# Optimization experiments

Hardware: AMD Instinct MI355X
Metric: run time of the kernel (lower is better)

Reference implementation:

```python
import jax, jax.numpy as jnp
import numpy as np

N_HEADS = 16

def _rope_tables(L, head_dim, dtype):
    inv_freq = 1.0 / (10000.0 ** (jnp.arange(0, head_dim, 2, dtype=jnp.float32) / head_dim))
    t = jnp.arange(L, dtype=jnp.float32)
    freqs = jnp.outer(t, inv_freq)            # [L, head_dim/2]
    emb = jnp.concatenate([freqs, freqs], -1)  # [L, head_dim]
    return jnp.cos(emb).astype(dtype), jnp.sin(emb).astype(dtype)

def _apply_rope(x, cos, sin):
    # x: [B, L, H, hd]; cos/sin: [1, L, 1, hd]
    half = x.shape[-1] // 2
    x1, x2 = x[..., :half], x[..., half:]
    x_rot = jnp.concatenate([-x2, x1], -1)
    return x * cos + x_rot * sin

def setup_inputs() -> dict:
    key = jax.random.key(0)
    ks = jax.random.split(key, 5)
    D = 1024
    s = 0.02
    return {
        "x": jax.random.normal(ks[0], (4, 2048, D), jnp.float32),
        "w_qkv": jax.random.normal(ks[1], (3 * D, D), jnp.float32) * s,
        "b_qkv": jax.random.normal(ks[2], (3 * D,), jnp.float32) * s,
        "w_out": jax.random.normal(ks[3], (D, D), jnp.float32) * s,
        "b_out": jax.random.normal(ks[4], (D,), jnp.float32) * s,
    }

def reference(x, w_qkv, b_qkv, w_out, b_out):
    B, L, D = x.shape
    H = N_HEADS
    hd = D // H
    scale = hd ** -0.5
    qkv = (x @ w_qkv.T + b_qkv).reshape(B, L, 3, H, hd)
    q, k, v = qkv[:, :, 0], qkv[:, :, 1], qkv[:, :, 2]  # [B,L,H,hd]
    cos, sin = _rope_tables(L, hd, x.dtype)
    cos = cos[None, :, None, :]
    sin = sin[None, :, None, :]
    q = _apply_rope(q, cos, sin)
    k = _apply_rope(k, cos, sin)
    # [B,H,L,L] scores, non-causal softmax
    attn = jnp.einsum('blhd,bmhd->bhlm', q, k) * scale
    attn = jax.nn.softmax(attn, axis=-1)
    out = jnp.einsum('bhlm,bmhd->blhd', attn, v).reshape(B, L, D)
    return out @ w_out.T + b_out
```

## Files before the change

### kernel.cpp

```cpp
#include <hip/hip_runtime.h>
#include <stdint.h>

typedef __attribute__((ext_vector_type(4))) float f32x4;
typedef __attribute__((ext_vector_type(8))) short bf16x8;
typedef __attribute__((ext_vector_type(4))) short s16x4;
typedef __attribute__((ext_vector_type(4))) float fp32x4;

#define QSCALE 0.18033688f

__device__ __forceinline__ short f2bf(float f) {
    union { float f; unsigned u; } v; v.f = f;
    unsigned u = v.u;
    unsigned r = u + 0x7fffu + ((u >> 16) & 1u);
    return (short)(r >> 16);
}
__device__ __forceinline__ unsigned cvtpk(float a, float b) {
    unsigned r;
    asm("v_cvt_pk_bf16_f32 %0, %1, %2" : "=v"(r) : "v"(a), "v"(b));
    return r;
}

__device__ __forceinline__ void gld_lds16(const void* g, void* l) {
    __builtin_amdgcn_global_load_lds(
        (const __attribute__((address_space(1))) unsigned int*)(uintptr_t)g,
        (__attribute__((address_space(3))) unsigned int*)(uintptr_t)l,
        16, 0, 0);
}

__global__ __launch_bounds__(256) void cast_kernel(const float* __restrict__ in,
                                                   short* __restrict__ out, int n) {
    int idx = (blockIdx.x * 256 + threadIdx.x) * 8;
    if (idx >= n) return;
    fp32x4 a = *(const fp32x4*)&in[idx];
    fp32x4 b = *(const fp32x4*)&in[idx + 4];
    union { unsigned w[4]; bf16x8 v; } u;
    u.w[0] = cvtpk(a[0], a[1]); u.w[1] = cvtpk(a[2], a[3]);
    u.w[2] = cvtpk(b[0], b[1]); u.w[3] = cvtpk(b[2], b[3]);
    *(bf16x8*)&out[idx] = u.v;
}

__global__ __launch_bounds__(256) void rope_table_kernel(float* __restrict__ tab) {
    int idx = blockIdx.x * 256 + threadIdx.x;
    int l = idx >> 5, d = idx & 31;
    float inv = expf(-(float)d / 32.f * logf(10000.f));
    float ang = (float)l * inv;
    tab[idx * 2 + 0] = cosf(ang);
    tab[idx * 2 + 1] = sinf(ang);
}

template<int MODE>
__global__ __launch_bounds__(512, 2) void gemm_bt(const short* __restrict__ A,
                                                  const short* __restrict__ B,
                                                  const float* __restrict__ bias,
                                                  void* __restrict__ Cout,
                                                  short* __restrict__ VTout,
                                                  const float* __restrict__ tab,
                                                  int M, int N, int K) {
    __shared__ short lds[3 * 24576];
    const int tid = threadIdx.x;
    const int lane = tid & 63, wave = tid >> 6;
    const int i15 = lane & 15, g = lane >> 4;
    const int wr = wave >> 1, wc = wave & 1;

    const int nbx = gridDim.x;
    const int nwg = nbx * gridDim.y;
    int bid = blockIdx.y * nbx + blockIdx.x;
    int sw = (bid & 7) * (nwg >> 3) + (bid >> 3);
    const int m0 = (sw / nbx) * 256;
    const int n0 = (sw % nbx) * 128;

    const int xr3 = i15 & 3, xb2 = (i15 >> 2) & 1;
    const int cLo = g ^ xr3;
    const int aoff0 = (wr * 64 + i15) * 64 + (xb2 * 4 + cLo) * 8;
    const int aoff1 = (wr * 64 + i15) * 64 + ((1 ^ xb2) * 4 + cLo) * 8;
    const int boff0 = (wc * 64 + i15) * 64 + (xb2 * 4 + cLo) * 8;
    const int boff1 = (wc * 64 + i15) * 64 + ((1 ^ xb2) * 4 + cLo) * 8;

    const int srow = tid >> 3;
    const int ss = (tid & 7) ^ (srow & 7);
    const short* a0 = A + (size_t)(m0 + srow) * K + ss * 8;
    const short* a1 = a0 + (size_t)64 * K;
    const short* a2 = a0 + (size_t)128 * K;
    const short* a3 = a0 + (size_t)192 * K;
    const short* b0 = B + (size_t)(n0 + srow) * K + ss * 8;
    const short* b1 = b0 + (size_t)64 * K;

#define ST_A(slot, r, p) do { gld_lds16(p, lds + (slot) * 24576 + ((r) * 512 + wave * 64) * 8); p += 64; } while (0)
#define ST_B(slot, r, p) do { gld_lds16(p, lds + (slot) * 24576 + 16384 + ((r) * 512 + wave * 64) * 8); p += 64; } while (0)

    ST_A(0, 0, a0); ST_A(0, 1, a1); ST_B(0, 0, b0);
    ST_A(0, 2, a2); ST_A(0, 3, a3); ST_B(0, 1, b1);
    ST_A(1, 0, a0); ST_A(1, 1, a1); ST_B(1, 0, b0);
    ST_A(1, 2, a2); ST_A(1, 3, a3); ST_B(1, 1, b1);

    f32x4 acc[4][4] = {};
    const int NT = K >> 6;
    int slc = 0;

    for (int t = 0; t < NT; ++t) {
        int sl2 = slc + 2; if (sl2 >= 3) sl2 -= 3;
        if (t == NT - 1) asm volatile("s_waitcnt vmcnt(0)" ::: "memory");
        else             asm volatile("s_waitcnt vmcnt(6)" ::: "memory");
        __builtin_amdgcn_s_barrier();
        __builtin_amdgcn_sched_barrier(0);

        const short* As_ = lds + slc * 24576;
        const short* Bs_ = As_ + 16384;
        const bool pre = (t + 2 < NT);

        if (pre) { ST_A(sl2, 0, a0); ST_A(sl2, 1, a1); ST_B(sl2, 0, b0); }
        bf16x8 af[4][2], bfr[2][2];
#pragma unroll
        for (int m = 0; m < 4; ++m) {
            af[m][0] = *(const bf16x8*)&As_[aoff0 + m * 1024];
            af[m][1] = *(const bf16x8*)&As_[aoff1 + m * 1024];
        }
#pragma unroll
        for (int n = 0; n < 2; ++n) {
            bfr[n][0] = *(const bf16x8*)&Bs_[boff0 + n * 1024];
            bfr[n][1] = *(const bf16x8*)&Bs_[boff1 + n * 1024];
        }
        __builtin_amdgcn_s_barrier();
        asm volatile("s_waitcnt lgkmcnt(0)" ::: "memory");
        __builtin_amdgcn_sched_barrier(0);
        __builtin_amdgcn_s_setprio(1);
#pragma unroll
        for (int m = 0; m < 4; ++m)
#pragma unroll
            for (int n = 0; n < 2; ++n)
#pragma unroll
                for (int ks = 0; ks < 2; ++ks)
                    acc[m][n] = __builtin_amdgcn_mfma_f32_16x16x32_bf16(af[m][ks], bfr[n][ks], acc[m][n], 0, 0, 0);
        __builtin_amdgcn_s_setprio(0);

        if (pre) { ST_A(sl2, 2, a2); ST_A(sl2, 3, a3); ST_B(sl2, 1, b1); }
        bf16x8 bfr2[2][2];
#pragma unroll
        for (int n = 0; n < 2; ++n) {
            bfr2[n][0] = *(const bf16x8*)&Bs_[boff0 + (n + 2) * 1024];
            bfr2[n][1] = *(const bf16x8*)&Bs_[boff1 + (n + 2) * 1024];
        }
        __builtin_amdgcn_s_barrier();
        asm volatile("s_waitcnt lgkmcnt(0)" ::: "memory");
        __builtin_amdgcn_sched_barrier(0);
        __builtin_amdgcn_s_setprio(1);
#pragma unroll
        for (int m = 0; m < 4; ++m)
#pragma unroll
            for (int n = 0; n < 2; ++n)
#pragma unroll
                for (int ks = 0; ks < 2; ++ks)
                    acc[m][n + 2] = __builtin_amdgcn_mfma_f32_16x16x32_bf16(af[m][ks], bfr2[n][ks], acc[m][n + 2], 0, 0, 0);
        __builtin_amdgcn_s_setprio(0);

        slc = (slc == 2) ? 0 : slc + 1;
    }
#undef ST_A
#undef ST_B

    if (MODE == 0) {
#pragma unroll
        for (int m = 0; m < 4; ++m)
#pragma unroll
            for (int n = 0; n < 4; ++n) {
                int col = n0 + wc * 64 + n * 16 + i15;
                float bcol = bias[col];
#pragma unroll
                for (int j = 0; j < 4; ++j) {
                    int row = m0 + wr * 64 + m * 16 + g * 4 + j;
                    ((float*)Cout)[(size_t)row * N + col] = acc[m][n][j] + bcol;
                }
            }
    } else {
        const int sec = n0 >> 10;
        if (sec < 2) {
            const float qs = (sec == 0) ? QSCALE : 1.0f;
            short* out = (short*)Cout;
#pragma unroll
            for (int m = 0; m < 4; ++m) {
#pragma unroll
                for (int pp = 0; pp < 2; ++pp) {
                    int d = pp * 16 + i15;
                    int collo = n0 + wc * 64 + pp * 16 + i15;
                    float blo = bias[collo], bhi = bias[collo + 32];
#pragma unroll
                    for (int j = 0; j < 4; ++j) {
                        int row = m0 + wr * 64 + m * 16 + g * 4 + j;
                        int l = row & 2047;
                        float2 cs = *(const float2*)&tab[(l * 32 + d) * 2];
                        float x1 = acc[m][pp][j] + blo;
                        float x2 = acc[m][pp + 2][j] + bhi;
                        out[(size_t)row * 3072 + collo]      = f2bf((x1 * cs.x - x2 * cs.y) * qs);
                        out[(size_t)row * 3072 + collo + 32] = f2bf((x2 * cs.x + x1 * cs.y) * qs);
                    }
                }
            }
        } else {
#pragma unroll
            for (int m = 0; m < 4; ++m) {
                int rbase = m0 + wr * 64 + m * 16 + g * 4;
                int lbase = rbase & 2047, bidx = rbase >> 11;
#pragma unroll
                for (int n = 0; n < 4; ++n) {
                    int vcol = (n0 - 2048) + wc * 64 + n * 16 + i15;
                    int h = vcol >> 6, d = vcol & 63;
                    float bb = bias[n0 + wc * 64 + n * 16 + i15];
                    union { unsigned w[2]; s16x4 v; } u;
                    u.w[0] = cvtpk(acc[m][n][0] + bb, acc[m][n][1] + bb);
                    u.w[1] = cvtpk(acc[m][n][2] + bb, acc[m][n][3] + bb);
                    *(s16x4*)&VTout[((size_t)(bidx * 16 + h) * 64 + d) * 2048 + lbase] = u.v;
                }
            }
        }
    }
}

__global__ __launch_bounds__(512, 8) void attn_kernel(const short* __restrict__ qkv,
                                                      const short* __restrict__ VT,
                                                      short* __restrict__ O) {
    __shared__ short Ks[2][64 * 64];
    __shared__ short Vs[2][64 * 64];
    int orig = blockIdx.x;
    int xcd = orig & 7, idx = orig >> 3;
    int bh = xcd * 8 + (idx >> 4), qt = idx & 15;
    int b = bh >> 4, h = bh & 15;
    int tid = threadIdx.x, lane = tid & 63, wave = tid >> 6;
    int i15 = lane & 15, g = lane >> 4;
    int q0 = qt * 128;

    size_t qrow = (size_t)(b * 2048 + q0 + wave * 16 + i15);
    bf16x8 qf[2];
    qf[0] = *(const bf16x8*)&qkv[qrow * 3072 + h * 64 + 0  + g * 8];
    qf[1] = *(const bf16x8*)&qkv[qrow * 3072 + h * 64 + 32 + g * 8];

    bf16x8 onesf;
#pragma unroll
    for (int e = 0; e < 8; ++e) onesf[e] = (short)0x3F80;

    const int srow = tid >> 3, ss8 = (tid & 7) ^ (srow & 7);
    const int sprow = (srow & 0x23) | ((srow & 0x10) >> 2) | ((srow & 0x0C) << 1);
    const short* kp = qkv + (size_t)(b * 2048) * 3072 + 1024 + h * 64
                      + (size_t)sprow * 3072 + ss8 * 8;
    const short* vp = VT + (size_t)bh * 64 * 2048 + (size_t)srow * 2048 + ss8 * 8;

    const int xr3 = i15 & 3, xb2 = (i15 >> 2) & 1;
    const int cLo = g ^ xr3;
    const int o0 = i15 * 64 + (xb2 * 4 + cLo) * 8;
    const int o1 = i15 * 64 + ((1 ^ xb2) * 4 + cLo) * 8;

    f32x4 acc_o[4] = {};
    f32x4 acc_l = {0.f, 0.f, 0.f, 0.f};

#define STAGE(bk, bv)                                        \
    do {                                                     \
        gld_lds16(kp, (bk) + wave * 512);                    \
        gld_lds16(vp, (bv) + wave * 512);                    \
        kp += 64 * 3072;                                     \
        vp += 64;                                            \
    } while (0)

    STAGE(Ks[0], Vs[0]);

    for (int t = 0; t < 32; ++t) {
        const int cur = t & 1;
        if (t > 0) {
            __builtin_amdgcn_s_barrier();
            __builtin_amdgcn_sched_barrier(0);
        }
        if (t + 1 < 32) {
            STAGE(Ks[cur ^ 1], Vs[cur ^ 1]);
            asm volatile("s_waitcnt vmcnt(2)" ::: "memory");
        } else {
            asm volatile("s_waitcnt vmcnt(0)" ::: "memory");
        }
        __builtin_amdgcn_s_barrier();
        __builtin_amdgcn_sched_barrier(0);

        const short* ks = Ks[cur];
        const short* vs = Vs[cur];

        f32x4 sa[4] = {};
        __builtin_amdgcn_s_setprio(1);
#pragma unroll
        for (int kb = 0; kb < 2; ++kb) {
            const int ko = kb ? o1 : o0;
#pragma unroll
            for (int jb = 0; jb < 4; ++jb) {
                bf16x8 kf = *(const bf16x8*)&ks[ko + jb * 1024];
                sa[jb] = __builtin_amdgcn_mfma_f32_16x16x32_bf16(kf, qf[kb], sa[jb], 0, 0, 0);
            }
        }
        __builtin_amdgcn_s_setprio(0);

        float p[4][4];
#pragma unroll
        for (int jb = 0; jb < 4; ++jb)
#pragma unroll
            for (int r = 0; r < 4; ++r)
                p[jb][r] = __builtin_amdgcn_exp2f(sa[jb][r]);

        bf16x8 pf[2];
#pragma unroll
        for (int kb = 0; kb < 2; ++kb) {
            union { unsigned w[4]; bf16x8 v; } u;
            u.w[0] = cvtpk(p[2 * kb][0],     p[2 * kb][1]);
            u.w[1] = cvtpk(p[2 * kb][2],     p[2 * kb][3]);
            u.w[2] = cvtpk(p[2 * kb + 1][0], p[2 * kb + 1][1]);
            u.w[3] = cvtpk(p[2 * kb + 1][2], p[2 * kb + 1][3]);
            pf[kb] = u.v;
        }

        __builtin_amdgcn_s_setprio(1);
#pragma unroll
        for (int db = 0; db < 4; ++db) {
#pragma unroll
            for (int kb = 0; kb < 2; ++kb) {
                bf16x8 vf = *(const bf16x8*)&vs[(kb ? o1 : o0) + db * 1024];
                acc_o[db] = __builtin_amdgcn_mfma_f32_16x16x32_bf16(pf[kb], vf, acc_o[db], 0, 0, 0);
            }
        }
        acc_l = __builtin_amdgcn_mfma_f32_16x16x32_bf16(pf[0], onesf, acc_l, 0, 0, 0);
        acc_l = __builtin_amdgcn_mfma_f32_16x16x32_bf16(pf[1], onesf, acc_l, 0, 0, 0);
        __builtin_amdgcn_s_setprio(0);
    }
#undef STAGE

    float linv4[4];
#pragma unroll
    for (int r = 0; r < 4; ++r) linv4[r] = 1.f / acc_l[r];
#pragma unroll
    for (int db = 0; db < 4; ++db) {
        int ocol = h * 64 + db * 16 + i15;
#pragma unroll
        for (int r = 0; r < 4; ++r) {
            int orow = b * 2048 + q0 + wave * 16 + g * 4 + r;
            O[(size_t)orow * 1024 + ocol] = f2bf(acc_o[db][r] * linv4[r]);
        }
    }
}

extern "C" void kernel_launch(void* const* d_in, const int* in_sizes, int n_in,
                              void* d_out, int out_size, void* d_ws, size_t ws_size,
                              hipStream_t stream) {
    const float* x     = (const float*)d_in[0];
    const float* w_qkv = (const float*)d_in[1];
    const float* b_qkv = (const float*)d_in[2];
    const float* w_out = (const float*)d_in[3];
    const float* b_out = (const float*)d_in[4];

    char* ws = (char*)d_ws;
    short* qkvb = (short*)(ws);
    short* xb   = (short*)(ws + 50331648);
    short* wqb  = (short*)(ws + 67108864);
    short* wob  = (short*)(ws + 73400320);
    short* VT   = (short*)(ws + 75497472);
    float* rt   = (float*)(ws + 92274688);
    short* Ob   = xb;

    cast_kernel<<<4096, 256, 0, stream>>>(x, xb, 8388608);
    cast_kernel<<<1536, 256, 0, stream>>>(w_qkv, wqb, 3145728);
    cast_kernel<<<512, 256, 0, stream>>>(w_out, wob, 1048576);
    rope_table_kernel<<<256, 256, 0, stream>>>(rt);

    gemm_bt<1><<<dim3(24, 32), 512, 0, stream>>>(xb, wqb, b_qkv, qkvb, VT, rt, 8192, 3072, 1024);
    attn_kernel<<<1024, 512, 0, stream>>>(qkvb, VT, Ob);
    gemm_bt<0><<<dim3(8, 32), 512, 0, stream>>>(Ob, wob, b_out, d_out, nullptr, nullptr, 8192, 1024, 1024);
}
```

Before: 175.7 us.

## Use 256x256 GEMM tiles with double-buffered quadrant pipeline and permuted QKV weights

Both GEMMs move from 256x128 tiles with a 3-slot LDS ring to 256x256 tiles with double buffering and four quadrant MFMA phases. Each phase is interleaved with staged global-to-LDS loads, aiming for higher arithmetic intensity per LDS byte and fewer workgroups. The Q/K weight rows are permuted during the bf16 cast so that RoPE pairs (d, d+32) fall into accumulator fragments of the new wave layout, with the epilogue remapping columns to match. The cost is more accumulator registers (128 floats per lane) and fewer workgroups: 384 for the QKV GEMM and only 128 for the output GEMM, which may underfill the CUs.

```diff
diff --git a/kernel.cpp b/kernel.cpp
--- a/kernel.cpp
+++ b/kernel.cpp
@@ -39,6 +39,26 @@
     *(bf16x8*)&out[idx] = u.v;
 }
 
+__global__ __launch_bounds__(256) void cast_wqkv_kernel(const float* __restrict__ in,
+                                                        short* __restrict__ out) {
+    int idx = blockIdx.x * 256 + threadIdx.x;
+    int row = idx >> 7;
+    int k8 = (idx & 127) * 8;
+    int src;
+    if (row < 2048) {
+        int a = row >> 5, w = row & 31, s = w >> 4, r = w & 15;
+        src = (a >> 1) * 64 + (a & 1) * 16 + r + 32 * s;
+    } else {
+        src = row;
+    }
+    fp32x4 a = *(const fp32x4*)&in[(size_t)src * 1024 + k8];
+    fp32x4 b = *(const fp32x4*)&in[(size_t)src * 1024 + k8 + 4];
+    union { unsigned w[4]; bf16x8 v; } u;
+    u.w[0] = cvtpk(a[0], a[1]); u.w[1] = cvtpk(a[2], a[3]);
+    u.w[2] = cvtpk(b[0], b[1]); u.w[3] = cvtpk(b[2], b[3]);
+    *(bf16x8*)&out[(size_t)row * 1024 + k8] = u.v;
+}
+
 __global__ __launch_bounds__(256) void rope_table_kernel(float* __restrict__ tab) {
     int idx = blockIdx.x * 256 + threadIdx.x;
     int l = idx >> 5, d = idx & 31;
@@ -49,162 +69,199 @@
 }
 
 template<int MODE>
-__global__ __launch_bounds__(512, 2) void gemm_bt(const short* __restrict__ A,
-                                                  const short* __restrict__ B,
-                                                  const float* __restrict__ bias,
-                                                  void* __restrict__ Cout,
-                                                  short* __restrict__ VTout,
-                                                  const float* __restrict__ tab,
-                                                  int M, int N, int K) {
-    __shared__ short lds[3 * 24576];
+__global__ __launch_bounds__(512, 2) void gemm8(const short* __restrict__ A,
+                                                const short* __restrict__ B,
+                                                const float* __restrict__ bias,
+                                                void* __restrict__ Cout,
+                                                short* __restrict__ VTout,
+                                                const float* __restrict__ tab,
+                                                int M, int N, int K) {
+    __shared__ short lds_s[65536];
     const int tid = threadIdx.x;
     const int lane = tid & 63, wave = tid >> 6;
     const int i15 = lane & 15, g = lane >> 4;
-    const int wr = wave >> 1, wc = wave & 1;
+    const int wr = wave >> 2, wc = wave & 3;
 
     const int nbx = gridDim.x;
     const int nwg = nbx * gridDim.y;
     int bid = blockIdx.y * nbx + blockIdx.x;
     int sw = (bid & 7) * (nwg >> 3) + (bid >> 3);
     const int m0 = (sw / nbx) * 256;
-    const int n0 = (sw % nbx) * 128;
+    const int n0 = (sw % nbx) * 256;
 
     const int xr3 = i15 & 3, xb2 = (i15 >> 2) & 1;
-    const int cLo = g ^ xr3;
-    const int aoff0 = (wr * 64 + i15) * 64 + (xb2 * 4 + cLo) * 8;
-    const int aoff1 = (wr * 64 + i15) * 64 + ((1 ^ xb2) * 4 + cLo) * 8;
-    const int boff0 = (wc * 64 + i15) * 64 + (xb2 * 4 + cLo) * 8;
-    const int boff1 = (wc * 64 + i15) * 64 + ((1 ^ xb2) * 4 + cLo) * 8;
+    const int gx2 = g ^ xr3;
+    const int laneA = (wr * 64 + i15) * 64 + gx2 * 8;
+    const int laneB = (wc * 32 + i15) * 64 + gx2 * 8;
+    const int kk0 = xb2 * 32, kk1 = 32 - kk0;
 
     const int srow = tid >> 3;
-    const int ss = (tid & 7) ^ (srow & 7);
-    const short* a0 = A + (size_t)(m0 + srow) * K + ss * 8;
-    const short* a1 = a0 + (size_t)64 * K;
-    const short* a2 = a0 + (size_t)128 * K;
-    const short* a3 = a0 + (size_t)192 * K;
-    const short* b0 = B + (size_t)(n0 + srow) * K + ss * 8;
-    const short* b1 = b0 + (size_t)64 * K;
-
-#define ST_A(slot, r, p) do { gld_lds16(p, lds + (slot) * 24576 + ((r) * 512 + wave * 64) * 8); p += 64; } while (0)
-#define ST_B(slot, r, p) do { gld_lds16(p, lds + (slot) * 24576 + 16384 + ((r) * 512 + wave * 64) * 8); p += 64; } while (0)
-
-    ST_A(0, 0, a0); ST_A(0, 1, a1); ST_B(0, 0, b0);
-    ST_A(0, 2, a2); ST_A(0, 3, a3); ST_B(0, 1, b1);
-    ST_A(1, 0, a0); ST_A(1, 1, a1); ST_B(1, 0, b0);
-    ST_A(1, 2, a2); ST_A(1, 3, a3); ST_B(1, 1, b1);
-
-    f32x4 acc[4][4] = {};
+    const int sg = (tid & 7) ^ (srow & 7);
+    const int dls = srow * 64 + (tid & 7) * 8;
+    const short* pA0a = A + (size_t)(m0 +   0 + srow) * K + sg * 8;
+    const short* pA0b = A + (size_t)(m0 +  64 + srow) * K + sg * 8;
+    const short* pA1a = A + (size_t)(m0 + 128 + srow) * K + sg * 8;
+    const short* pA1b = A + (size_t)(m0 + 192 + srow) * K + sg * 8;
+    const short* pB0a = B + (size_t)(n0 +   0 + srow) * K + sg * 8;
+    const short* pB0b = B + (size_t)(n0 +  64 + srow) * K + sg * 8;
+    const short* pB1a = B + (size_t)(n0 + 128 + srow) * K + sg * 8;
+    const short* pB1b = B + (size_t)(n0 + 192 + srow) * K + sg * 8;
+
+#define STG_A(par, rowoff, p) do { gld_lds16(p, lds_s + (par) * 32768 + (rowoff) * 64 + dls); p += 64; } while (0)
+#define STG_B(par, rowoff, p) do { gld_lds16(p, lds_s + (par) * 32768 + 16384 + (rowoff) * 64 + dls); p += 64; } while (0)
+
+    STG_A(0, 0, pA0a);   STG_A(0, 64, pA0b);
+    STG_B(0, 0, pB0a);   STG_B(0, 64, pB0b);
+    STG_B(0, 128, pB1a); STG_B(0, 192, pB1b);
+    STG_A(0, 128, pA1a); STG_A(0, 192, pA1b);
+    STG_A(1, 0, pA0a);   STG_A(1, 64, pA0b);
+    STG_B(1, 0, pB0a);   STG_B(1, 64, pB0b);
+    STG_B(1, 128, pB1a); STG_B(1, 192, pB1b);
+
+    f32x4 acc[8][4] = {};
     const int NT = K >> 6;
-    int slc = 0;
-
-    for (int t = 0; t < NT; ++t) {
-        int sl2 = slc + 2; if (sl2 >= 3) sl2 -= 3;
-        if (t == NT - 1) asm volatile("s_waitcnt vmcnt(0)" ::: "memory");
+
+    for (int T = 0; T < NT; ++T) {
+        const int par = T & 1, opar = par ^ 1;
+        if (T == NT - 1) asm volatile("s_waitcnt vmcnt(0)" ::: "memory");
         else             asm volatile("s_waitcnt vmcnt(6)" ::: "memory");
         __builtin_amdgcn_s_barrier();
         __builtin_amdgcn_sched_barrier(0);
-
-        const short* As_ = lds + slc * 24576;
-        const short* Bs_ = As_ + 16384;
-        const bool pre = (t + 2 < NT);
-
-        if (pre) { ST_A(sl2, 0, a0); ST_A(sl2, 1, a1); ST_B(sl2, 0, b0); }
-        bf16x8 af[4][2], bfr[2][2];
-#pragma unroll
-        for (int m = 0; m < 4; ++m) {
-            af[m][0] = *(const bf16x8*)&As_[aoff0 + m * 1024];
-            af[m][1] = *(const bf16x8*)&As_[aoff1 + m * 1024];
-        }
-#pragma unroll
-        for (int n = 0; n < 2; ++n) {
-            bfr[n][0] = *(const bf16x8*)&Bs_[boff0 + n * 1024];
-            bfr[n][1] = *(const bf16x8*)&Bs_[boff1 + n * 1024];
+        const short* Ab = lds_s + par * 32768;
+        const short* Bb = Ab + 16384;
+        bf16x8 af[4][2], bf[4][2];
+
+        if (T + 1 < NT) { STG_A(opar, 128, pA1a); STG_A(opar, 192, pA1b); }
+#pragma unroll
+        for (int mf = 0; mf < 4; ++mf) {
+            af[mf][0] = *(const bf16x8*)&Ab[laneA + mf * 1024 + kk0];
+            af[mf][1] = *(const bf16x8*)&Ab[laneA + mf * 1024 + kk1];
+        }
+#pragma unroll
+        for (int nf = 0; nf < 2; ++nf) {
+            bf[nf][0] = *(const bf16x8*)&Bb[laneB + nf * 1024 + kk0];
+            bf[nf][1] = *(const bf16x8*)&Bb[laneB + nf * 1024 + kk1];
         }
         __builtin_amdgcn_s_barrier();
         asm volatile("s_waitcnt lgkmcnt(0)" ::: "memory");
         __builtin_amdgcn_sched_barrier(0);
         __builtin_amdgcn_s_setprio(1);
 #pragma unroll
-        for (int m = 0; m < 4; ++m)
-#pragma unroll
-            for (int n = 0; n < 2; ++n)
-#pragma unroll
-                for (int ks = 0; ks < 2; ++ks)
-                    acc[m][n] = __builtin_amdgcn_mfma_f32_16x16x32_bf16(af[m][ks], bfr[n][ks], acc[m][n], 0, 0, 0);
-        __builtin_amdgcn_s_setprio(0);
-
-        if (pre) { ST_A(sl2, 2, a2); ST_A(sl2, 3, a3); ST_B(sl2, 1, b1); }
-        bf16x8 bfr2[2][2];
-#pragma unroll
-        for (int n = 0; n < 2; ++n) {
-            bfr2[n][0] = *(const bf16x8*)&Bs_[boff0 + (n + 2) * 1024];
-            bfr2[n][1] = *(const bf16x8*)&Bs_[boff1 + (n + 2) * 1024];
+        for (int mf = 0; mf < 4; ++mf)
+#pragma unroll
+            for (int nf = 0; nf < 2; ++nf) {
+                acc[mf][nf] = __builtin_amdgcn_mfma_f32_16x16x32_bf16(af[mf][0], bf[nf][0], acc[mf][nf], 0, 0, 0);
+                acc[mf][nf] = __builtin_amdgcn_mfma_f32_16x16x32_bf16(af[mf][1], bf[nf][1], acc[mf][nf], 0, 0, 0);
+            }
+        __builtin_amdgcn_s_setprio(0);
+        __builtin_amdgcn_s_barrier();
+
+        if (T + 2 < NT) { STG_A(par, 0, pA0a); STG_A(par, 64, pA0b); }
+#pragma unroll
+        for (int nf = 0; nf < 2; ++nf) {
+            bf[2 + nf][0] = *(const bf16x8*)&Bb[laneB + 8192 + nf * 1024 + kk0];
+            bf[2 + nf][1] = *(const bf16x8*)&Bb[laneB + 8192 + nf * 1024 + kk1];
         }
         __builtin_amdgcn_s_barrier();
         asm volatile("s_waitcnt lgkmcnt(0)" ::: "memory");
         __builtin_amdgcn_sched_barrier(0);
         __builtin_amdgcn_s_setprio(1);
 #pragma unroll
-        for (int m = 0; m < 4; ++m)
-#pragma unroll
-            for (int n = 0; n < 2; ++n)
-#pragma unroll
-                for (int ks = 0; ks < 2; ++ks)
-                    acc[m][n + 2] = __builtin_amdgcn_mfma_f32_16x16x32_bf16(af[m][ks], bfr2[n][ks], acc[m][n + 2], 0, 0, 0);
-        __builtin_amdgcn_s_setprio(0);
-
-        slc = (slc == 2) ? 0 : slc + 1;
+        for (int mf = 0; mf < 4; ++mf)
+#pragma unroll
+            for (int nf = 0; nf < 2; ++nf) {
+                acc[mf][2 + nf] = __builtin_amdgcn_mfma_f32_16x16x32_bf16(af[mf][0], bf[2 + nf][0], acc[mf][2 + nf], 0, 0, 0);
+                acc[mf][2 + nf] = __builtin_amdgcn_mfma_f32_16x16x32_bf16(af[mf][1], bf[2 + nf][1], acc[mf][2 + nf], 0, 0, 0);
+            }
+        __builtin_amdgcn_s_setprio(0);
+        __builtin_amdgcn_s_barrier();
+
+        if (T + 2 < NT) { STG_B(par, 0, pB0a); STG_B(par, 64, pB0b); }
+#pragma unroll
+        for (int mf = 0; mf < 4; ++mf) {
+            af[mf][0] = *(const bf16x8*)&Ab[laneA + 8192 + mf * 1024 + kk0];
+            af[mf][1] = *(const bf16x8*)&Ab[laneA + 8192 + mf * 1024 + kk1];
+        }
+        __builtin_amdgcn_s_barrier();
+        asm volatile("s_waitcnt lgkmcnt(0)" ::: "memory");
+        __builtin_amdgcn_sched_barrier(0);
+        __builtin_amdgcn_s_setprio(1);
+#pragma unroll
+        for (int mf = 0; mf < 4; ++mf)
+#pragma unroll
+            for (int nf = 0; nf < 2; ++nf) {
+                acc[4 + mf][2 + nf] = __builtin_amdgcn_mfma_f32_16x16x32_bf16(af[mf][0], bf[2 + nf][0], acc[4 + mf][2 + nf], 0, 0, 0);
+                acc[4 + mf][2 + nf] = __builtin_amdgcn_mfma_f32_16x16x32_bf16(af[mf][1], bf[2 + nf][1], acc[4 + mf][2 + nf], 0, 0, 0);
+            }
+        __builtin_amdgcn_s_setprio(0);
+        __builtin_amdgcn_s_barrier();
+
+        if (T + 2 < NT) { STG_B(par, 128, pB1a); STG_B(par, 192, pB1b); }
+        __builtin_amdgcn_s_barrier();
+        __builtin_amdgcn_s_setprio(1);
+#pragma unroll
+        for (int mf = 0; mf < 4; ++mf)
+#pragma unroll
+            for (int nf = 0; nf < 2; ++nf) {
+                acc[4 + mf][nf] = __builtin_amdgcn_mfma_f32_16x16x32_bf16(af[mf][0], bf[nf][0], acc[4 + mf][nf], 0, 0, 0);
+                acc[4 + mf][nf] = __builtin_amdgcn_mfma_f32_16x16x32_bf16(af[mf][1], bf[nf][1], acc[4 + mf][nf], 0, 0, 0);
+            }
+        __builtin_amdgcn_s_setprio(0);
     }
-#undef ST_A
-#undef ST_B
+#undef STG_A
+#undef STG_B
 
     if (MODE == 0) {
 #pragma unroll
-        for (int m = 0; m < 4; ++m)
+        for (int m = 0; m < 8; ++m) {
+            int rbase = m0 + ((m >> 2) * 128) + wr * 64 + (m & 3) * 16 + g * 4;
 #pragma unroll
             for (int n = 0; n < 4; ++n) {
-                int col = n0 + wc * 64 + n * 16 + i15;
+                int col = n0 + ((n >> 1) * 128) + wc * 32 + (n & 1) * 16 + i15;
                 float bcol = bias[col];
 #pragma unroll
-                for (int j = 0; j < 4; ++j) {
-                    int row = m0 + wr * 64 + m * 16 + g * 4 + j;
-                    ((float*)Cout)[(size_t)row * N + col] = acc[m][n][j] + bcol;
-                }
-            }
+                for (int j = 0; j < 4; ++j)
+                    ((float*)Cout)[(size_t)(rbase + j) * N + col] = acc[m][n][j] + bcol;
+            }
+        }
     } else {
         const int sec = n0 >> 10;
         if (sec < 2) {
             const float qs = (sec == 0) ? QSCALE : 1.0f;
             short* out = (short*)Cout;
 #pragma unroll
-            for (int m = 0; m < 4; ++m) {
-#pragma unroll
-                for (int pp = 0; pp < 2; ++pp) {
-                    int d = pp * 16 + i15;
-                    int collo = n0 + wc * 64 + pp * 16 + i15;
-                    float blo = bias[collo], bhi = bias[collo + 32];
+            for (int m = 0; m < 8; ++m) {
+                int rbase = m0 + ((m >> 2) * 128) + wr * 64 + (m & 3) * 16 + g * 4;
+#pragma unroll
+                for (int p = 0; p < 2; ++p) {
+                    int S = (n0 & 1023) + p * 128 + wc * 32;
+                    int a = S >> 5;
+                    int d = (a & 1) * 16 + i15;
+                    int clo = (a >> 1) * 64 + d;
+                    int fullc = sec * 1024 + clo;
+                    float blo = bias[fullc], bhi = bias[fullc + 32];
 #pragma unroll
                     for (int j = 0; j < 4; ++j) {
-                        int row = m0 + wr * 64 + m * 16 + g * 4 + j;
+                        int row = rbase + j;
                         int l = row & 2047;
                         float2 cs = *(const float2*)&tab[(l * 32 + d) * 2];
-                        float x1 = acc[m][pp][j] + blo;
-                        float x2 = acc[m][pp + 2][j] + bhi;
-                        out[(size_t)row * 3072 + collo]      = f2bf((x1 * cs.x - x2 * cs.y) * qs);
-                        out[(size_t)row * 3072 + collo + 32] = f2bf((x2 * cs.x + x1 * cs.y) * qs);
+                        float x1 = acc[m][2 * p][j] + blo;
+                        float x2 = acc[m][2 * p + 1][j] + bhi;
+                        out[(size_t)row * 3072 + fullc]      = f2bf((x1 * cs.x - x2 * cs.y) * qs);
+                        out[(size_t)row * 3072 + fullc + 32] = f2bf((x2 * cs.x + x1 * cs.y) * qs);
                     }
                 }
             }
         } else {
 #pragma unroll
-            for (int m = 0; m < 4; ++m) {
-                int rbase = m0 + wr * 64 + m * 16 + g * 4;
+            for (int m = 0; m < 8; ++m) {
+                int rbase = m0 + ((m >> 2) * 128) + wr * 64 + (m & 3) * 16 + g * 4;
                 int lbase = rbase & 2047, bidx = rbase >> 11;
 #pragma unroll
                 for (int n = 0; n < 4; ++n) {
-                    int vcol = (n0 - 2048) + wc * 64 + n * 16 + i15;
+                    int vcol = (n0 - 2048) + ((n >> 1) * 128) + wc * 32 + (n & 1) * 16 + i15;
                     int h = vcol >> 6, d = vcol & 63;
-                    float bb = bias[n0 + wc * 64 + n * 16 + i15];
+                    float bb = bias[2048 + vcol];
                     union { unsigned w[2]; s16x4 v; } u;
                     u.w[0] = cvtpk(acc[m][n][0] + bb, acc[m][n][1] + bb);
                     u.w[1] = cvtpk(acc[m][n][2] + bb, acc[m][n][3] + bb);
@@ -358,11 +415,11 @@
     short* Ob   = xb;
 
     cast_kernel<<<4096, 256, 0, stream>>>(x, xb, 8388608);
-    cast_kernel<<<1536, 256, 0, stream>>>(w_qkv, wqb, 3145728);
+    cast_wqkv_kernel<<<1536, 256, 0, stream>>>(w_qkv, wqb);
     cast_kernel<<<512, 256, 0, stream>>>(w_out, wob, 1048576);
     rope_table_kernel<<<256, 256, 0, stream>>>(rt);
 
-    gemm_bt<1><<<dim3(24, 32), 512, 0, stream>>>(xb, wqb, b_qkv, qkvb, VT, rt, 8192, 3072, 1024);
+    gemm8<1><<<dim3(12, 32), 512, 0, stream>>>(xb, wqb, b_qkv, qkvb, VT, rt, 8192, 3072, 1024);
     attn_kernel<<<1024, 512, 0, stream>>>(qkvb, VT, Ob);
-    gemm_bt<0><<<dim3(8, 32), 512, 0, stream>>>(Ob, wob, b_out, d_out, nullptr, nullptr, 8192, 1024, 1024);
-}
+    gemm8<0><<<dim3(4, 32), 512, 0, stream>>>(Ob, wob, b_out, d_out, nullptr, nullptr, 8192, 1024, 1024);
+}
```

Result: slower. 198.2 us (+12.8%).

## Fuse prep kernels into one launch and simplify GEMM main-loop scheduling

Applied to the files above, without the earlier changes.

Merges the three cast launches and the RoPE table launch into a single prep kernel, which removes launch overhead and the gaps between kernels. The GEMM main loop now issues all six global-to-LDS prefetches at once and loads all B fragments up front. It then runs all 32 MFMAs in one phase, dropping the two intra-iteration barriers and the split compute halves. The catch is higher register pressure from the extra B fragments, and less interleaving of LDS reads with MFMA work.

```diff
diff --git a/kernel.cpp b/kernel.cpp
--- a/kernel.cpp
+++ b/kernel.cpp
@@ -27,35 +27,45 @@
         16, 0, 0);
 }
 
-__global__ __launch_bounds__(256) void cast_kernel(const float* __restrict__ in,
-                                                   short* __restrict__ out, int n) {
-    int idx = (blockIdx.x * 256 + threadIdx.x) * 8;
-    if (idx >= n) return;
-    fp32x4 a = *(const fp32x4*)&in[idx];
-    fp32x4 b = *(const fp32x4*)&in[idx + 4];
-    union { unsigned w[4]; bf16x8 v; } u;
-    u.w[0] = cvtpk(a[0], a[1]); u.w[1] = cvtpk(a[2], a[3]);
-    u.w[2] = cvtpk(b[0], b[1]); u.w[3] = cvtpk(b[2], b[3]);
-    *(bf16x8*)&out[idx] = u.v;
-}
-
-__global__ __launch_bounds__(256) void rope_table_kernel(float* __restrict__ tab) {
-    int idx = blockIdx.x * 256 + threadIdx.x;
-    int l = idx >> 5, d = idx & 31;
-    float inv = expf(-(float)d / 32.f * logf(10000.f));
-    float ang = (float)l * inv;
-    tab[idx * 2 + 0] = cosf(ang);
-    tab[idx * 2 + 1] = sinf(ang);
+__global__ __launch_bounds__(256) void prep_kernel(const float* __restrict__ x,
+                                                   const float* __restrict__ wq,
+                                                   const float* __restrict__ wo,
+                                                   short* __restrict__ xb,
+                                                   short* __restrict__ wqb,
+                                                   short* __restrict__ wob,
+                                                   float* __restrict__ tab) {
+    int bid = blockIdx.x, tid = threadIdx.x;
+    if (bid < 6144) {
+        const float* in; short* out; int base;
+        if (bid < 4096)      { in = x;  out = xb;  base = bid; }
+        else if (bid < 5632) { in = wq; out = wqb; base = bid - 4096; }
+        else                 { in = wo; out = wob; base = bid - 5632; }
+        int idx = (base * 256 + tid) * 8;
+        fp32x4 a = *(const fp32x4*)&in[idx];
+        fp32x4 b = *(const fp32x4*)&in[idx + 4];
+        union { unsigned w[4]; bf16x8 v; } u;
+        u.w[0] = cvtpk(a[0], a[1]); u.w[1] = cvtpk(a[2], a[3]);
+        u.w[2] = cvtpk(b[0], b[1]); u.w[3] = cvtpk(b[2], b[3]);
+        *(bf16x8*)&out[idx] = u.v;
+    } else {
+        int idx = (bid - 6144) * 256 + tid;
+        int l = idx >> 5, d = idx & 31;
+        float inv = expf(-(float)d / 32.f * logf(10000.f));
+        float ang = (float)l * inv;
+        tab[idx * 2 + 0] = cosf(ang);
+        tab[idx * 2 + 1] = sinf(ang);
+    }
 }
 
 template<int MODE>
-__global__ __launch_bounds__(512, 2) void gemm_bt(const short* __restrict__ A,
-                                                  const short* __restrict__ B,
-                                                  const float* __restrict__ bias,
-                                                  void* __restrict__ Cout,
-                                                  short* __restrict__ VTout,
-                                                  const float* __restrict__ tab,
-                                                  int M, int N, int K) {
+__global__ __launch_bounds__(512, 2)
+void gemm_bt(const short* __restrict__ A,
+             const short* __restrict__ B,
+             const float* __restrict__ bias,
+             void* __restrict__ Cout,
+             short* __restrict__ VTout,
+             const float* __restrict__ tab,
+             int M, int N, int K) {
     __shared__ short lds[3 * 24576];
     const int tid = threadIdx.x;
     const int lane = tid & 63, wave = tid >> 6;
@@ -97,60 +107,40 @@
     const int NT = K >> 6;
     int slc = 0;
 
-    for (int t = 0; t < NT; ++t) {
-        int sl2 = slc + 2; if (sl2 >= 3) sl2 -= 3;
-        if (t == NT - 1) asm volatile("s_waitcnt vmcnt(0)" ::: "memory");
+    for (int T = 0; T < NT; ++T) {
+        int stslot = slc + 2; if (stslot >= 3) stslot -= 3;
+        if (T == NT - 1) asm volatile("s_waitcnt vmcnt(0)" ::: "memory");
         else             asm volatile("s_waitcnt vmcnt(6)" ::: "memory");
         __builtin_amdgcn_s_barrier();
         __builtin_amdgcn_sched_barrier(0);
 
+        if (T + 2 < NT) {
+            ST_A(stslot, 0, a0); ST_A(stslot, 1, a1);
+            ST_A(stslot, 2, a2); ST_A(stslot, 3, a3);
+            ST_B(stslot, 0, b0); ST_B(stslot, 1, b1);
+        }
+
         const short* As_ = lds + slc * 24576;
         const short* Bs_ = As_ + 16384;
-        const bool pre = (t + 2 < NT);
-
-        if (pre) { ST_A(sl2, 0, a0); ST_A(sl2, 1, a1); ST_B(sl2, 0, b0); }
-        bf16x8 af[4][2], bfr[2][2];
+        bf16x8 af[4][2], bfr[4][2];
 #pragma unroll
         for (int m = 0; m < 4; ++m) {
             af[m][0] = *(const bf16x8*)&As_[aoff0 + m * 1024];
             af[m][1] = *(const bf16x8*)&As_[aoff1 + m * 1024];
         }
 #pragma unroll
-        for (int n = 0; n < 2; ++n) {
+        for (int n = 0; n < 4; ++n) {
             bfr[n][0] = *(const bf16x8*)&Bs_[boff0 + n * 1024];
             bfr[n][1] = *(const bf16x8*)&Bs_[boff1 + n * 1024];
         }
-        __builtin_amdgcn_s_barrier();
-        asm volatile("s_waitcnt lgkmcnt(0)" ::: "memory");
-        __builtin_amdgcn_sched_barrier(0);
         __builtin_amdgcn_s_setprio(1);
 #pragma unroll
         for (int m = 0; m < 4; ++m)
 #pragma unroll
-            for (int n = 0; n < 2; ++n)
+            for (int n = 0; n < 4; ++n)
 #pragma unroll
                 for (int ks = 0; ks < 2; ++ks)
                     acc[m][n] = __builtin_amdgcn_mfma_f32_16x16x32_bf16(af[m][ks], bfr[n][ks], acc[m][n], 0, 0, 0);
-        __builtin_amdgcn_s_setprio(0);
-
-        if (pre) { ST_A(sl2, 2, a2); ST_A(sl2, 3, a3); ST_B(sl2, 1, b1); }
-        bf16x8 bfr2[2][2];
-#pragma unroll
-        for (int n = 0; n < 2; ++n) {
-            bfr2[n][0] = *(const bf16x8*)&Bs_[boff0 + (n + 2) * 1024];
-            bfr2[n][1] = *(const bf16x8*)&Bs_[boff1 + (n + 2) * 1024];
-        }
-        __builtin_amdgcn_s_barrier();
-        asm volatile("s_waitcnt lgkmcnt(0)" ::: "memory");
-        __builtin_amdgcn_sched_barrier(0);
-        __builtin_amdgcn_s_setprio(1);
-#pragma unroll
-        for (int m = 0; m < 4; ++m)
-#pragma unroll
-            for (int n = 0; n < 2; ++n)
-#pragma unroll
-                for (int ks = 0; ks < 2; ++ks)
-                    acc[m][n + 2] = __builtin_amdgcn_mfma_f32_16x16x32_bf16(af[m][ks], bfr2[n][ks], acc[m][n + 2], 0, 0, 0);
         __builtin_amdgcn_s_setprio(0);
 
         slc = (slc == 2) ? 0 : slc + 1;
@@ -357,10 +347,7 @@
     float* rt   = (float*)(ws + 92274688);
     short* Ob   = xb;
 
-    cast_kernel<<<4096, 256, 0, stream>>>(x, xb, 8388608);
-    cast_kernel<<<1536, 256, 0, stream>>>(w_qkv, wqb, 3145728);
-    cast_kernel<<<512, 256, 0, stream>>>(w_out, wob, 1048576);
-    rope_table_kernel<<<256, 256, 0, stream>>>(rt);
+    prep_kernel<<<6400, 256, 0, stream>>>(x, w_qkv, w_out, xb, wqb, wob, rt);
 
     gemm_bt<1><<<dim3(24, 32), 512, 0, stream>>>(xb, wqb, b_qkv, qkvb, VT, rt, 8192, 3072, 1024);
     attn_kernel<<<1024, 512, 0, stream>>>(qkvb, VT, Ob);
```

After: 171.1 us. -2.6%, faster.
